# Kernel tuning notes

Hardware: AMD Instinct MI355X
Metric: run time of the kernel (lower is better)

## Reference

```python
import jax, jax.numpy as jnp
import numpy as np

N = 50000      # num_nodes
E = 800000     # num_edges
D_IN = 128
D_HID = 128
D_EMB = 128
G = 4          # num_gcns
BN_EPS = 1e-5


def setup_inputs() -> dict:
    key = jax.random.key(0)
    ks = jax.random.split(key, 8)
    x = jax.random.normal(ks[0], (N, D_IN), dtype=jnp.float32)
    edge_index = jax.random.randint(ks[1], (2, E), 0, N, dtype=jnp.int64)
    # per-GCN params, stacked on leading G axis
    W1 = jax.random.normal(ks[2], (G, D_IN, D_HID), dtype=jnp.float32) / np.sqrt(D_IN)
    b1 = jnp.zeros((G, D_HID), dtype=jnp.float32)
    W2 = jax.random.normal(ks[3], (G, D_HID, D_EMB), dtype=jnp.float32) / np.sqrt(D_HID)
    b2 = jnp.zeros((G, D_EMB), dtype=jnp.float32)
    gamma1 = jnp.ones((G, D_HID), dtype=jnp.float32)
    beta1 = jnp.zeros((G, D_HID), dtype=jnp.float32)
    gamma2 = jnp.ones((G, D_EMB), dtype=jnp.float32)
    beta2 = jnp.zeros((G, D_EMB), dtype=jnp.float32)
    alpha = jnp.asarray(0.25, dtype=jnp.float32)  # PReLU (single shared param)
    mix_embed = jnp.full((N, G), 1.0 / G, dtype=jnp.float32)
    return {"x": x, "edge_index": edge_index, "W1": W1, "b1": b1, "W2": W2,
            "b2": b2, "gamma1": gamma1, "beta1": beta1, "gamma2": gamma2,
            "beta2": beta2, "alpha": alpha, "mix_embed": mix_embed}


def _gcn_norm(edge_index, num_nodes):
    # PyG GCNConv: add self-loops, symmetric normalization D^-1/2 (A+I) D^-1/2
    row, col = edge_index[0], edge_index[1]
    loop = jnp.arange(num_nodes, dtype=edge_index.dtype)
    row = jnp.concatenate([row, loop])
    col = jnp.concatenate([col, loop])
    w = jnp.ones(row.shape[0], dtype=jnp.float32)
    deg = jax.ops.segment_sum(w, col, num_segments=num_nodes)
    dinv = jnp.where(deg > 0, deg ** -0.5, 0.0)
    norm = dinv[row] * w * dinv[col]
    return row, col, norm


def _propagate(h, row, col, norm, num_nodes):
    # gather from source, scale by edge norm, scatter-add to target
    msg = h[row] * norm[:, None]
    return jax.ops.segment_sum(msg, col, num_segments=num_nodes)


def _batchnorm(z, gamma, beta):
    mu = jnp.mean(z, axis=0)
    var = jnp.mean((z - mu) ** 2, axis=0)  # biased, as torch BN training mode
    return (z - mu) * jax.lax.rsqrt(var + BN_EPS) * gamma + beta


def _prelu(z, alpha):
    return jnp.where(z > 0, z, alpha * z)


def reference(x, edge_index, W1, b1, W2, b2, gamma1, beta1, gamma2, beta2, alpha, mix_embed):
    num_nodes = x.shape[0]
    row, col, norm = _gcn_norm(edge_index, num_nodes)
    mix = jax.nn.softmax(mix_embed, axis=-1)  # [N, G]
    out = jnp.zeros((num_nodes, D_EMB), dtype=x.dtype)
    for g in range(G):  # small fixed number of mixture components
        h = x @ W1[g]
        z = _propagate(h, row, col, norm, num_nodes) + b1[g]
        z = _prelu(_batchnorm(z, gamma1[g], beta1[g]), alpha)
        h = z @ W2[g]
        z = _propagate(h, row, col, norm, num_nodes) + b2[g]
        z = _prelu(_batchnorm(z, gamma2[g], beta2[g]), alpha)
        out = out + mix[:, g:g + 1] * z
    return out
```

## Files before the change

kernel.cpp:

```cpp
#include <hip/hip_runtime.h>
#include <stdint.h>

static constexpr float EPS = 1e-5f;
static constexpr int XB = 64;

typedef __attribute__((ext_vector_type(8))) short bfrag;
typedef __attribute__((ext_vector_type(4))) float ffrag;

__device__ __forceinline__ float bf2f(unsigned short u){
  union { unsigned int i; float f; } v; v.i = ((unsigned int)u) << 16; return v.f;
}
__device__ __forceinline__ unsigned short f2bf(float f){
  union { float f; unsigned int i; } v; v.f = f;
  unsigned int x = v.i;
  x += 0x7fffu + ((x >> 16) & 1u);
  return (unsigned short)(x >> 16);
}
__device__ __forceinline__ float lo16(unsigned int v){ return bf2f((unsigned short)(v & 0xffffu)); }
__device__ __forceinline__ float hi16(unsigned int v){ return bf2f((unsigned short)(v >> 16)); }
__device__ __forceinline__ unsigned int pack2(float a, float b){
  return ((unsigned int)f2bf(b) << 16) | (unsigned int)f2bf(a);
}

__global__ __launch_bounds__(256) void k_deg(const int* __restrict__ col, int* __restrict__ indeg,
                                             int N, int E, int dbl,
                                             const float* __restrict__ W1, const float* __restrict__ W2,
                                             unsigned short* __restrict__ Wt1, unsigned short* __restrict__ Wt2){
  int b = blockIdx.x;
  if (b < dbl){
    int e0 = (b * 256 + threadIdx.x) * 2;
    if (e0 < E){
      if (e0 + 1 < E){
        int2 cc = *(const int2*)&col[e0];
        unsigned c0 = (unsigned)cc.x, c1 = (unsigned)cc.y;
        if (c0 < (unsigned)N) atomicAdd(&indeg[c0], 1);
        if (c1 < (unsigned)N) atomicAdd(&indeg[c1], 1);
      } else {
        unsigned c0 = (unsigned)col[e0];
        if (c0 < (unsigned)N) atomicAdd(&indeg[c0], 1);
      }
    }
  } else {
    int idx = (b - dbl) * 256 + threadIdx.x;
    const float* W = W1; unsigned short* Wt = Wt1;
    if (idx >= 65536){ idx -= 65536; W = W2; Wt = Wt2; }
    int c = idx >> 7, k = idx & 127;
    int g = c >> 7, j = c & 127;
    Wt[(size_t)c * 128 + k] = f2bf(W[(size_t)g*16384 + k*128 + j]);
  }
}

__global__ void k_alloc(const int* __restrict__ indeg, int* __restrict__ ctr,
                        int* __restrict__ offs, int* __restrict__ cursor,
                        float* __restrict__ dinv, int N){
  int tid = blockIdx.x * 256 + threadIdx.x;
  int lane = threadIdx.x & 63;
  int v = (tid < N) ? indeg[tid] : 0;
  int incl = v;
  #pragma unroll
  for (int d = 1; d < 64; d <<= 1){
    int u = __shfl_up(incl, d);
    if (lane >= d) incl += u;
  }
  int base = 0;
  if (lane == 63) base = atomicAdd(ctr, incl);
  base = __shfl(base, 63);
  if (tid < N){
    int o = base + incl - v;
    offs[tid] = o; cursor[tid] = o;
    dinv[tid] = rsqrtf((float)(v + 1));
  }
}

__global__ __launch_bounds__(256) void k_scatter(const int* __restrict__ row, const int* __restrict__ col,
                                                 int* __restrict__ cursor, int* __restrict__ csr,
                                                 int N, int E, int sbl,
                                                 const float* __restrict__ x, const float* __restrict__ dinv,
                                                 unsigned short* __restrict__ xs, int total4x){
  int b = blockIdx.x;
  if (b < sbl){
    int e0 = (b * 256 + threadIdx.x) * 2;
    #pragma unroll
    for (int q = 0; q < 2; q++){
      int e = e0 + q;
      if (e < E){
        unsigned c = (unsigned)col[e];
        if (c < (unsigned)N){
          int p = atomicAdd(&cursor[c], 1);
          unsigned r = (unsigned)row[e];
          csr[p] = (r < (unsigned)N) ? (int)r : 0;
        }
      }
    }
  } else {
    int idx = (b - sbl) * 256 + threadIdx.x;
    int stride = (gridDim.x - sbl) * 256;
    for (; idx < total4x; idx += stride){
      int i = idx >> 5;
      float di = dinv[i];
      float4 v = ((const float4*)x)[idx];
      ushort4 o;
      o.x = f2bf(di * v.x); o.y = f2bf(di * v.y);
      o.z = f2bf(di * v.z); o.w = f2bf(di * v.w);
      ((ushort4*)xs)[idx] = o;
    }
  }
}

__global__ __launch_bounds__(256) void k_prop_x(const unsigned int* __restrict__ xs2,
                                               const int* __restrict__ csr,
                                               const int* __restrict__ offs, const int* __restrict__ indeg,
                                               const float* __restrict__ dinv,
                                               unsigned int* __restrict__ s2, int N){
  int i = blockIdx.x * 4 + (threadIdx.x >> 6);
  if (i >= N) return;
  int c2 = threadIdx.x & 63;
  unsigned int sv = xs2[(size_t)i*64 + c2];
  float ax = lo16(sv), ay = hi16(sv);
  int e = offs[i], end = e + indeg[i];
  for (; e + 16 <= end; e += 16){
    int r[16];
    #pragma unroll
    for (int j = 0; j < 16; j++) r[j] = csr[e + j];
    unsigned int v[16];
    #pragma unroll
    for (int j = 0; j < 16; j++) v[j] = xs2[(size_t)r[j]*64 + c2];
    #pragma unroll
    for (int j = 0; j < 16; j++){ ax += lo16(v[j]); ay += hi16(v[j]); }
  }
  for (; e + 4 <= end; e += 4){
    int r0 = csr[e], r1 = csr[e+1], r2 = csr[e+2], r3 = csr[e+3];
    unsigned int v0 = xs2[(size_t)r0*64 + c2], v1 = xs2[(size_t)r1*64 + c2];
    unsigned int v2 = xs2[(size_t)r2*64 + c2], v3 = xs2[(size_t)r3*64 + c2];
    ax += lo16(v0)+lo16(v1)+lo16(v2)+lo16(v3);
    ay += hi16(v0)+hi16(v1)+hi16(v2)+hi16(v3);
  }
  for (; e < end; e++){
    unsigned int v = xs2[(size_t)csr[e]*64 + c2];
    ax += lo16(v); ay += hi16(v);
  }
  float di = dinv[i];
  s2[(size_t)i*64 + c2] = pack2(di * ax, di * ay);
}

__global__ __launch_bounds__(256) void k_gram(const unsigned short* __restrict__ in,
                                              int rstride, int coff128,
                                              float* __restrict__ Gpart, float* __restrict__ msumbase,
                                              int N){
  int gy = blockIdx.y;
  const unsigned short* src = in + gy * coff128;
  float* Gp = Gpart + ((size_t)gy * XB + blockIdx.x) * 16384;
  float* msum = msumbase + gy * 128;

  __shared__ unsigned short st[128 * 40];
  __shared__ float colsum[128];

  int t = threadIdx.x;
  int wv = t >> 6, lane = t & 63, l16 = lane & 15, quad = lane >> 4;
  if (t < 128) colsum[t] = 0.f;

  int sn = t & 31, scb = t >> 5;

  ffrag acc[2][8];
  #pragma unroll
  for (int a = 0; a < 2; a++)
    #pragma unroll
    for (int b = 0; b < 8; b++) acc[a][b] = (ffrag){0.f,0.f,0.f,0.f};

  float cs[16];
  #pragma unroll
  for (int j = 0; j < 16; j++) cs[j] = 0.f;

  for (int c0 = blockIdx.x * 32; c0 < N; c0 += gridDim.x * 32){
    __syncthreads();
    int n = c0 + sn;
    ushort4 u0, u1, u2, u3;
    if (n < N){
      const ushort4* p = (const ushort4*)(src + (size_t)n * rstride + scb * 16);
      u0 = p[0]; u1 = p[1]; u2 = p[2]; u3 = p[3];
    } else {
      u0 = u1 = u2 = u3 = (ushort4){0,0,0,0};
    }
    unsigned short vals[16] = {u0.x,u0.y,u0.z,u0.w, u1.x,u1.y,u1.z,u1.w,
                               u2.x,u2.y,u2.z,u2.w, u3.x,u3.y,u3.z,u3.w};
    #pragma unroll
    for (int j = 0; j < 16; j++){
      st[(scb * 16 + j) * 40 + sn] = vals[j];
      cs[j] += bf2f(vals[j]);
    }
    __syncthreads();
    #pragma unroll
    for (int ta = 0; ta < 2; ta++){
      int ra = wv * 2 + ta;
      bfrag af = *(const bfrag*)&st[(ra * 16 + l16) * 40 + quad * 8];
      #pragma unroll
      for (int tb = 0; tb < 8; tb++){
        bfrag bf = *(const bfrag*)&st[(tb * 16 + l16) * 40 + quad * 8];
        acc[ta][tb] = __builtin_amdgcn_mfma_f32_16x16x32_bf16(af, bf, acc[ta][tb], 0, 0, 0);
      }
    }
  }
  #pragma unroll
  for (int j = 0; j < 16; j++) atomicAdd(&colsum[scb * 16 + j], cs[j]);
  __syncthreads();
  if (t < 128) atomicAdd(&msum[t], colsum[t]);
  #pragma unroll
  for (int ta = 0; ta < 2; ta++){
    #pragma unroll
    for (int tb = 0; tb < 8; tb++){
      int row0 = wv * 32 + ta * 16 + quad * 4;
      int colg = tb * 16 + l16;
      #pragma unroll
      for (int r = 0; r < 4; r++)
        Gp[(size_t)(row0 + r) * 128 + colg] = acc[ta][tb][r];
    }
  }
}

__global__ __launch_bounds__(256) void k_gred(const float* __restrict__ Gpart, float* __restrict__ G){
  int i = blockIdx.x * 256 + threadIdx.x;
  int grp = blockIdx.y;
  const float* src = Gpart + (size_t)grp * XB * 16384;
  float s = 0.f;
  #pragma unroll 4
  for (int xb = 0; xb < XB; xb++) s += src[(size_t)xb * 16384 + i];
  G[(size_t)grp * 16384 + i] = s;
}

__global__ __launch_bounds__(64) void k_bnfit(const float* __restrict__ W,
                                              const float* __restrict__ gamma, const float* __restrict__ beta,
                                              const float* __restrict__ Gbase, int gmul,
                                              const float* __restrict__ msumbase, int mmul,
                                              float* __restrict__ scale, float* __restrict__ shiftF,
                                              float invN){
  int c = blockIdx.x;
  int g = c >> 7, j = c & 127;
  const float* Wc = W + (size_t)g * 16384 + j;
  const float* G  = Gbase + (size_t)g * gmul;
  const float* mv = msumbase + g * mmul;
  __shared__ float wl[128];
  __shared__ float ml[128];
  int t = threadIdx.x;
  for (int k = t; k < 128; k += 64){ wl[k] = Wc[(size_t)k * 128]; ml[k] = mv[k] * invN; }
  __syncthreads();
  float quad = 0.f, dm = 0.f;
  #pragma unroll
  for (int kk = 0; kk < 2; kk++){
    int k = t + kk * 64;
    float wk = wl[k];
    dm += ml[k] * wk;
    const float* Gr = G + (size_t)k * 128;
    float p = 0.f;
    for (int jj = 0; jj < 128; jj += 4){
      float4 gg = *(const float4*)(Gr + jj);
      float4 ww = *(const float4*)(wl + jj);
      p += gg.x*ww.x + gg.y*ww.y + gg.z*ww.z + gg.w*ww.w;
    }
    quad += wk * p;
  }
  for (int o = 32; o > 0; o >>= 1){
    quad += __shfl_down(quad, o);
    dm   += __shfl_down(dm, o);
  }
  if (t == 0){
    float var = quad * invN - dm * dm;
    float sc = gamma[c] * rsqrtf(var + EPS);
    scale[c] = sc;
    shiftF[c] = beta[c] - dm * sc;
  }
}

__global__ __launch_bounds__(256) void k_mm1f(const unsigned short* __restrict__ in,
                                              const unsigned short* __restrict__ Wt,
                                              const float* __restrict__ scale, const float* __restrict__ shiftF,
                                              const float* __restrict__ alpha_p, const float* __restrict__ dinv,
                                              unsigned short* __restrict__ h, int N){
  float alpha = alpha_p[0];
  int wave = threadIdx.x >> 6, lane = threadIdx.x & 63;
  int l16 = lane & 15, quad = lane >> 4;
  int node0 = blockIdx.x * 32 + l16;
  int node1 = node0 + 16;
  int nc0 = node0 < N ? node0 : N - 1;
  int nc1 = node1 < N ? node1 : N - 1;
  int colbase0 = wave * 128;
  float di0 = dinv[nc0], di1 = dinv[nc1];

  const unsigned short* ir0 = in + (size_t)nc0 * 128 + quad * 8;
  const unsigned short* ir1 = in + (size_t)nc1 * 128 + quad * 8;
  bfrag b0a = *(const bfrag*)(ir0),      b0b = *(const bfrag*)(ir1);
  bfrag b1a = *(const bfrag*)(ir0 + 32), b1b = *(const bfrag*)(ir1 + 32);
  bfrag b2a = *(const bfrag*)(ir0 + 64), b2b = *(const bfrag*)(ir1 + 64);
  bfrag b3a = *(const bfrag*)(ir0 + 96), b3b = *(const bfrag*)(ir1 + 96);

  #pragma unroll
  for (int ct = 0; ct < 8; ct++){
    int colbase = colbase0 + ct * 16;
    const unsigned short* wrow = Wt + (size_t)(colbase + l16) * 128 + quad * 8;
    bfrag a0 = *(const bfrag*)(wrow);
    bfrag a1 = *(const bfrag*)(wrow + 32);
    bfrag a2 = *(const bfrag*)(wrow + 64);
    bfrag a3 = *(const bfrag*)(wrow + 96);
    ffrag acc0 = {0.f,0.f,0.f,0.f}, acc1 = {0.f,0.f,0.f,0.f};
    acc0 = __builtin_amdgcn_mfma_f32_16x16x32_bf16(a0, b0a, acc0, 0, 0, 0);
    acc1 = __builtin_amdgcn_mfma_f32_16x16x32_bf16(a0, b0b, acc1, 0, 0, 0);
    acc0 = __builtin_amdgcn_mfma_f32_16x16x32_bf16(a1, b1a, acc0, 0, 0, 0);
    acc1 = __builtin_amdgcn_mfma_f32_16x16x32_bf16(a1, b1b, acc1, 0, 0, 0);
    acc0 = __builtin_amdgcn_mfma_f32_16x16x32_bf16(a2, b2a, acc0, 0, 0, 0);
    acc1 = __builtin_amdgcn_mfma_f32_16x16x32_bf16(a2, b2b, acc1, 0, 0, 0);
    acc0 = __builtin_amdgcn_mfma_f32_16x16x32_bf16(a3, b3a, acc0, 0, 0, 0);
    acc1 = __builtin_amdgcn_mfma_f32_16x16x32_bf16(a3, b3b, acc1, 0, 0, 0);
    int cb = colbase + quad * 4;
    float4 sc = *(const float4*)(scale + cb);
    float4 sh = *(const float4*)(shiftF + cb);
    float v0 = acc0[0]*sc.x + sh.x; v0 = v0 > 0.f ? v0 : alpha*v0;
    float v1 = acc0[1]*sc.y + sh.y; v1 = v1 > 0.f ? v1 : alpha*v1;
    float v2 = acc0[2]*sc.z + sh.z; v2 = v2 > 0.f ? v2 : alpha*v2;
    float v3 = acc0[3]*sc.w + sh.w; v3 = v3 > 0.f ? v3 : alpha*v3;
    float w0 = acc1[0]*sc.x + sh.x; w0 = w0 > 0.f ? w0 : alpha*w0;
    float w1 = acc1[1]*sc.y + sh.y; w1 = w1 > 0.f ? w1 : alpha*w1;
    float w2 = acc1[2]*sc.z + sh.z; w2 = w2 > 0.f ? w2 : alpha*w2;
    float w3 = acc1[3]*sc.w + sh.w; w3 = w3 > 0.f ? w3 : alpha*w3;
    uint2 o0, o1;
    o0.x = pack2(di0*v0, di0*v1); o0.y = pack2(di0*v2, di0*v3);
    o1.x = pack2(di1*w0, di1*w1); o1.y = pack2(di1*w2, di1*w3);
    if (node0 < N) *(uint2*)(h + (size_t)node0 * 512 + cb) = o0;
    if (node1 < N) *(uint2*)(h + (size_t)node1 * 512 + cb) = o1;
  }
}

__global__ __launch_bounds__(256) void k_prop_h(const unsigned int* __restrict__ h2,
                                                const int* __restrict__ csr,
                                                const int* __restrict__ offs, const int* __restrict__ indeg,
                                                const float* __restrict__ dinv,
                                                unsigned int* __restrict__ t2, int N, int coff){
  int i = blockIdx.x * 2 + (threadIdx.x >> 7);
  if (i >= N) return;
  int c2 = coff + (threadIdx.x & 127);
  unsigned int sv = h2[(size_t)i*256 + c2];
  float ax = lo16(sv), ay = hi16(sv);
  int e = offs[i], end = e + indeg[i];
  for (; e + 16 <= end; e += 16){
    int r[16];
    #pragma unroll
    for (int j = 0; j < 16; j++) r[j] = csr[e + j];
    unsigned int v[16];
    #pragma unroll
    for (int j = 0; j < 16; j++) v[j] = h2[(size_t)r[j]*256 + c2];
    #pragma unroll
    for (int j = 0; j < 16; j++){ ax += lo16(v[j]); ay += hi16(v[j]); }
  }
  for (; e + 4 <= end; e += 4){
    int r0 = csr[e], r1 = csr[e+1], r2 = csr[e+2], r3 = csr[e+3];
    unsigned int v0 = h2[(size_t)r0*256 + c2], v1 = h2[(size_t)r1*256 + c2];
    unsigned int v2 = h2[(size_t)r2*256 + c2], v3 = h2[(size_t)r3*256 + c2];
    ax += lo16(v0)+lo16(v1)+lo16(v2)+lo16(v3);
    ay += hi16(v0)+hi16(v1)+hi16(v2)+hi16(v3);
  }
  for (; e < end; e++){
    unsigned int v = h2[(size_t)csr[e]*256 + c2];
    ax += lo16(v); ay += hi16(v);
  }
  float di = dinv[i];
  t2[(size_t)i*256 + c2] = pack2(di * ax, di * ay);
}

__global__ __launch_bounds__(256) void k_mm2f(const unsigned short* __restrict__ t,
                                              const unsigned short* __restrict__ Wt,
                                              const float* __restrict__ scale, const float* __restrict__ shiftF,
                                              const float* __restrict__ alpha_p, const float* __restrict__ mixe,
                                              float* __restrict__ out, int N){
  __shared__ float red[4][16][132];
  float alpha = alpha_p[0];
  int wave = threadIdx.x >> 6, lane = threadIdx.x & 63;
  int l16 = lane & 15, quad = lane >> 4;
  int node = blockIdx.x * 16 + l16;
  int nc = node < N ? node : N - 1;

  float4 me = ((const float4*)mixe)[nc];
  float mx = fmaxf(fmaxf(me.x, me.y), fmaxf(me.z, me.w));
  float e0 = __expf(me.x - mx), e1 = __expf(me.y - mx), e2 = __expf(me.z - mx), e3 = __expf(me.w - mx);
  float inv = 1.f / (e0 + e1 + e2 + e3);
  float wvx = ((wave == 0) ? e0 : (wave == 1) ? e1 : (wave == 2) ? e2 : e3) * inv;

  const unsigned short* inrow = t + (size_t)nc * 512 + wave * 128 + quad * 8;
  bfrag b0 = *(const bfrag*)(inrow);
  bfrag b1 = *(const bfrag*)(inrow + 32);
  bfrag b2 = *(const bfrag*)(inrow + 64);
  bfrag b3 = *(const bfrag*)(inrow + 96);

  #pragma unroll
  for (int ct = 0; ct < 8; ct++){
    int c512 = wave * 128 + ct * 16;
    const unsigned short* wrow = Wt + (size_t)(c512 + l16) * 128 + quad * 8;
    bfrag a0 = *(const bfrag*)(wrow);
    bfrag a1 = *(const bfrag*)(wrow + 32);
    bfrag a2 = *(const bfrag*)(wrow + 64);
    bfrag a3 = *(const bfrag*)(wrow + 96);
    ffrag acc = {0.f, 0.f, 0.f, 0.f};
    acc = __builtin_amdgcn_mfma_f32_16x16x32_bf16(a0, b0, acc, 0, 0, 0);
    acc = __builtin_amdgcn_mfma_f32_16x16x32_bf16(a1, b1, acc, 0, 0, 0);
    acc = __builtin_amdgcn_mfma_f32_16x16x32_bf16(a2, b2, acc, 0, 0, 0);
    acc = __builtin_amdgcn_mfma_f32_16x16x32_bf16(a3, b3, acc, 0, 0, 0);
    int cb = c512 + quad * 4;
    float4 sc = *(const float4*)(scale + cb);
    float4 sh = *(const float4*)(shiftF + cb);
    float v0 = acc[0]*sc.x + sh.x; v0 = v0 > 0.f ? v0 : alpha*v0;
    float v1 = acc[1]*sc.y + sh.y; v1 = v1 > 0.f ? v1 : alpha*v1;
    float v2 = acc[2]*sc.z + sh.z; v2 = v2 > 0.f ? v2 : alpha*v2;
    float v3 = acc[3]*sc.w + sh.w; v3 = v3 > 0.f ? v3 : alpha*v3;
    int j = ct * 16 + quad * 4;
    float4 wr = {wvx*v0, wvx*v1, wvx*v2, wvx*v3};
    *(float4*)&red[wave][l16][j] = wr;
  }
  __syncthreads();
  int tt = threadIdx.x;
  int nn = tt >> 4, j0 = (tt & 15) * 8;
  int gnode = blockIdx.x * 16 + nn;
  if (gnode < N){
    float4 r0 = {0,0,0,0}, r1 = {0,0,0,0};
    #pragma unroll
    for (int w = 0; w < 4; w++){
      float4 p0 = *(const float4*)&red[w][nn][j0];
      float4 p1 = *(const float4*)&red[w][nn][j0 + 4];
      r0.x += p0.x; r0.y += p0.y; r0.z += p0.z; r0.w += p0.w;
      r1.x += p1.x; r1.y += p1.y; r1.z += p1.z; r1.w += p1.w;
    }
    float* op = out + (size_t)gnode * 128 + j0;
    *(float4*)(op) = r0;
    *(float4*)(op + 4) = r1;
  }
}

extern "C" void kernel_launch(void* const* d_in, const int* in_sizes, int n_in,
                              void* d_out, int out_size, void* d_ws, size_t ws_size,
                              hipStream_t stream) {
  const float* x      = (const float*)d_in[0];
  const int*   ei     = (const int*)d_in[1];
  const float* W1     = (const float*)d_in[2];
  const float* W2     = (const float*)d_in[4];
  const float* gamma1 = (const float*)d_in[6];
  const float* beta1  = (const float*)d_in[7];
  const float* gamma2 = (const float*)d_in[8];
  const float* beta2  = (const float*)d_in[9];
  const float* alpha  = (const float*)d_in[10];
  const float* mixe   = (const float*)d_in[11];
  float* out = (float*)d_out;

  const int N = in_sizes[0] / 128;
  const int E = in_sizes[1] / 2;
  const int* rowv = ei;
  const int* colv = ei + E;

  char* w = (char*)d_ws;
  size_t off = 0;
  auto take = [&](size_t bytes) -> void* {
    void* p = w + off;
    off = (off + bytes + 255) & ~(size_t)255;
    return p;
  };
  size_t zbeg = off;
  int*   indeg  = (int*)take((size_t)N * 4);
  int*   ctr    = (int*)take(256);
  float* m1     = (float*)take(512);
  float* m2     = (float*)take(2048);
  size_t zend = off;
  float* G1     = (float*)take(65536);
  float* G2     = (float*)take(262144);
  float* Gpart  = (float*)take((size_t)4 * XB * 16384 * 4);
  int*   cursor = (int*)take((size_t)N * 4);
  int*   offs   = (int*)take((size_t)N * 4);
  float* dinv   = (float*)take((size_t)N * 4);
  float* scale1 = (float*)take(2048);
  float* shift1 = (float*)take(2048);
  float* scale2 = (float*)take(2048);
  float* shift2 = (float*)take(2048);
  int*   csr    = (int*)take((size_t)E * 4);
  unsigned short* Wt1 = (unsigned short*)take(512 * 128 * 2);
  unsigned short* Wt2 = (unsigned short*)take(512 * 128 * 2);
  unsigned short* xs = (unsigned short*)take((size_t)N * 128 * 2);
  unsigned short* sb = (unsigned short*)take((size_t)N * 128 * 2);
  unsigned short* h  = (unsigned short*)take((size_t)N * 512 * 2);
  unsigned short* tb = (unsigned short*)take((size_t)N * 512 * 2);

  hipMemsetAsync((char*)d_ws + zbeg, 0, zend - zbeg, stream);

  int nb  = (N + 255) / 256;
  int dbl = (E + 511) / 512;
  float invN = 1.0f / (float)N;

  k_deg<<<dbl + 512, 256, 0, stream>>>(colv, indeg, N, E, dbl, W1, W2, Wt1, Wt2);
  k_alloc<<<nb, 256, 0, stream>>>(indeg, ctr, offs, cursor, dinv, N);
  k_scatter<<<dbl + 1024, 256, 0, stream>>>(rowv, colv, cursor, csr, N, E, dbl, x, dinv, xs, N * 32);

  k_prop_x<<<(N + 3) / 4, 256, 0, stream>>>((const unsigned int*)xs, csr, offs, indeg, dinv, (unsigned int*)sb, N);

  k_gram<<<dim3(XB, 1), 256, 0, stream>>>(sb, 128, 0, Gpart, m1, N);
  k_gred<<<dim3(64, 1), 256, 0, stream>>>(Gpart, G1);
  k_bnfit<<<512, 64, 0, stream>>>(W1, gamma1, beta1, G1, 0, m1, 0, scale1, shift1, invN);
  k_mm1f<<<(N + 31) / 32, 256, 0, stream>>>(sb, Wt1, scale1, shift1, alpha, dinv, h, N);

  k_prop_h<<<(N + 1) / 2, 256, 0, stream>>>((const unsigned int*)h, csr, offs, indeg, dinv, (unsigned int*)tb, N, 0);
  k_prop_h<<<(N + 1) / 2, 256, 0, stream>>>((const unsigned int*)h, csr, offs, indeg, dinv, (unsigned int*)tb, N, 128);

  k_gram<<<dim3(XB, 4), 256, 0, stream>>>(tb, 512, 128, Gpart, m2, N);
  k_gred<<<dim3(64, 4), 256, 0, stream>>>(Gpart, G2);
  k_bnfit<<<512, 64, 0, stream>>>(W2, gamma2, beta2, G2, 16384, m2, 128, scale2, shift2, invN);
  k_mm2f<<<(N + 15) / 16, 256, 0, stream>>>(tb, Wt2, scale2, shift2, alpha, mixe, out, N);
}
```

Measured before the change: 552.7 us.

## Privatize degree histogram and CSR cursors into 8 copies, merge prop_h launches

Degree counting and CSR scatter now use eight per-block-group private histograms and cursors, which spreads atomic contention across separate copies. The alloc kernel sums the copies, writes a total degree array, and derives a per-copy cursor base. Edge loads are widened to int4, four edges per thread. The two half-channel k_prop_h launches are replaced by one launch with one 256-thread block per node covering all 512 channels, trading more scratch memory and memset for fewer atomic collisions and launches.

```diff
diff --git a/kernel.cpp b/kernel.cpp
--- a/kernel.cpp
+++ b/kernel.cpp
@@ -28,16 +28,19 @@
                                              unsigned short* __restrict__ Wt1, unsigned short* __restrict__ Wt2){
   int b = blockIdx.x;
   if (b < dbl){
-    int e0 = (b * 256 + threadIdx.x) * 2;
-    if (e0 < E){
-      if (e0 + 1 < E){
-        int2 cc = *(const int2*)&col[e0];
-        unsigned c0 = (unsigned)cc.x, c1 = (unsigned)cc.y;
-        if (c0 < (unsigned)N) atomicAdd(&indeg[c0], 1);
-        if (c1 < (unsigned)N) atomicAdd(&indeg[c1], 1);
-      } else {
-        unsigned c0 = (unsigned)col[e0];
-        if (c0 < (unsigned)N) atomicAdd(&indeg[c0], 1);
+    int* hist = indeg + (size_t)(b & 7) * N;
+    int e0 = (b * 256 + threadIdx.x) * 4;
+    if (e0 + 4 <= E){
+      int4 cc = *(const int4*)&col[e0];
+      unsigned c0 = (unsigned)cc.x, c1 = (unsigned)cc.y, c2 = (unsigned)cc.z, c3 = (unsigned)cc.w;
+      if (c0 < (unsigned)N) atomicAdd(&hist[c0], 1);
+      if (c1 < (unsigned)N) atomicAdd(&hist[c1], 1);
+      if (c2 < (unsigned)N) atomicAdd(&hist[c2], 1);
+      if (c3 < (unsigned)N) atomicAdd(&hist[c3], 1);
+    } else {
+      for (int e = e0; e < E; e++){
+        unsigned c = (unsigned)col[e];
+        if (c < (unsigned)N) atomicAdd(&hist[c], 1);
       }
     }
   } else {
@@ -52,10 +55,18 @@
 
 __global__ void k_alloc(const int* __restrict__ indeg, int* __restrict__ ctr,
                         int* __restrict__ offs, int* __restrict__ cursor,
-                        float* __restrict__ dinv, int N){
+                        int* __restrict__ deg, float* __restrict__ dinv, int N){
   int tid = blockIdx.x * 256 + threadIdx.x;
   int lane = threadIdx.x & 63;
-  int v = (tid < N) ? indeg[tid] : 0;
+  int vs[8];
+  int v = 0;
+  if (tid < N){
+    #pragma unroll
+    for (int s = 0; s < 8; s++){ vs[s] = indeg[(size_t)s * N + tid]; v += vs[s]; }
+  } else {
+    #pragma unroll
+    for (int s = 0; s < 8; s++) vs[s] = 0;
+  }
   int incl = v;
   #pragma unroll
   for (int d = 1; d < 64; d <<= 1){
@@ -67,7 +78,11 @@
   base = __shfl(base, 63);
   if (tid < N){
     int o = base + incl - v;
-    offs[tid] = o; cursor[tid] = o;
+    offs[tid] = o;
+    deg[tid] = v;
+    int run = o;
+    #pragma unroll
+    for (int s = 0; s < 8; s++){ cursor[(size_t)s * N + tid] = run; run += vs[s]; }
     dinv[tid] = rsqrtf((float)(v + 1));
   }
 }
@@ -79,14 +94,26 @@
                                                  unsigned short* __restrict__ xs, int total4x){
   int b = blockIdx.x;
   if (b < sbl){
-    int e0 = (b * 256 + threadIdx.x) * 2;
-    #pragma unroll
-    for (int q = 0; q < 2; q++){
-      int e = e0 + q;
-      if (e < E){
+    int* cur = cursor + (size_t)(b & 7) * N;
+    int e0 = (b * 256 + threadIdx.x) * 4;
+    if (e0 + 4 <= E){
+      int4 cc = *(const int4*)&col[e0];
+      int4 rr = *(const int4*)&row[e0];
+      unsigned c0 = (unsigned)cc.x, c1 = (unsigned)cc.y, c2 = (unsigned)cc.z, c3 = (unsigned)cc.w;
+      int p0 = -1, p1 = -1, p2 = -1, p3 = -1;
+      if (c0 < (unsigned)N) p0 = atomicAdd(&cur[c0], 1);
+      if (c1 < (unsigned)N) p1 = atomicAdd(&cur[c1], 1);
+      if (c2 < (unsigned)N) p2 = atomicAdd(&cur[c2], 1);
+      if (c3 < (unsigned)N) p3 = atomicAdd(&cur[c3], 1);
+      if (p0 >= 0) csr[p0] = ((unsigned)rr.x < (unsigned)N) ? rr.x : 0;
+      if (p1 >= 0) csr[p1] = ((unsigned)rr.y < (unsigned)N) ? rr.y : 0;
+      if (p2 >= 0) csr[p2] = ((unsigned)rr.z < (unsigned)N) ? rr.z : 0;
+      if (p3 >= 0) csr[p3] = ((unsigned)rr.w < (unsigned)N) ? rr.w : 0;
+    } else {
+      for (int e = e0; e < E; e++){
         unsigned c = (unsigned)col[e];
         if (c < (unsigned)N){
-          int p = atomicAdd(&cursor[c], 1);
+          int p = atomicAdd(&cur[c], 1);
           unsigned r = (unsigned)row[e];
           csr[p] = (r < (unsigned)N) ? (int)r : 0;
         }
@@ -109,7 +136,7 @@
 
 __global__ __launch_bounds__(256) void k_prop_x(const unsigned int* __restrict__ xs2,
                                                const int* __restrict__ csr,
-                                               const int* __restrict__ offs, const int* __restrict__ indeg,
+                                               const int* __restrict__ offs, const int* __restrict__ deg,
                                                const float* __restrict__ dinv,
                                                unsigned int* __restrict__ s2, int N){
   int i = blockIdx.x * 4 + (threadIdx.x >> 6);
@@ -117,7 +144,7 @@
   int c2 = threadIdx.x & 63;
   unsigned int sv = xs2[(size_t)i*64 + c2];
   float ax = lo16(sv), ay = hi16(sv);
-  int e = offs[i], end = e + indeg[i];
+  int e = offs[i], end = e + deg[i];
   for (; e + 16 <= end; e += 16){
     int r[16];
     #pragma unroll
@@ -330,15 +357,14 @@
 
 __global__ __launch_bounds__(256) void k_prop_h(const unsigned int* __restrict__ h2,
                                                 const int* __restrict__ csr,
-                                                const int* __restrict__ offs, const int* __restrict__ indeg,
+                                                const int* __restrict__ offs, const int* __restrict__ deg,
                                                 const float* __restrict__ dinv,
-                                                unsigned int* __restrict__ t2, int N, int coff){
-  int i = blockIdx.x * 2 + (threadIdx.x >> 7);
-  if (i >= N) return;
-  int c2 = coff + (threadIdx.x & 127);
+                                                unsigned int* __restrict__ t2, int N){
+  int i = blockIdx.x;
+  int c2 = threadIdx.x;
   unsigned int sv = h2[(size_t)i*256 + c2];
   float ax = lo16(sv), ay = hi16(sv);
-  int e = offs[i], end = e + indeg[i];
+  int e = offs[i], end = e + deg[i];
   for (; e + 16 <= end; e += 16){
     int r[16];
     #pragma unroll
@@ -459,7 +485,7 @@
     return p;
   };
   size_t zbeg = off;
-  int*   indeg  = (int*)take((size_t)N * 4);
+  int*   indeg  = (int*)take((size_t)8 * N * 4);
   int*   ctr    = (int*)take(256);
   float* m1     = (float*)take(512);
   float* m2     = (float*)take(2048);
@@ -467,8 +493,9 @@
   float* G1     = (float*)take(65536);
   float* G2     = (float*)take(262144);
   float* Gpart  = (float*)take((size_t)4 * XB * 16384 * 4);
-  int*   cursor = (int*)take((size_t)N * 4);
+  int*   cursor = (int*)take((size_t)8 * N * 4);
   int*   offs   = (int*)take((size_t)N * 4);
+  int*   deg    = (int*)take((size_t)N * 4);
   float* dinv   = (float*)take((size_t)N * 4);
   float* scale1 = (float*)take(2048);
   float* shift1 = (float*)take(2048);
@@ -485,22 +512,21 @@
   hipMemsetAsync((char*)d_ws + zbeg, 0, zend - zbeg, stream);
 
   int nb  = (N + 255) / 256;
-  int dbl = (E + 511) / 512;
+  int dbl = (E + 1023) / 1024;
   float invN = 1.0f / (float)N;
 
   k_deg<<<dbl + 512, 256, 0, stream>>>(colv, indeg, N, E, dbl, W1, W2, Wt1, Wt2);
-  k_alloc<<<nb, 256, 0, stream>>>(indeg, ctr, offs, cursor, dinv, N);
+  k_alloc<<<nb, 256, 0, stream>>>(indeg, ctr, offs, cursor, deg, dinv, N);
   k_scatter<<<dbl + 1024, 256, 0, stream>>>(rowv, colv, cursor, csr, N, E, dbl, x, dinv, xs, N * 32);
 
-  k_prop_x<<<(N + 3) / 4, 256, 0, stream>>>((const unsigned int*)xs, csr, offs, indeg, dinv, (unsigned int*)sb, N);
+  k_prop_x<<<(N + 3) / 4, 256, 0, stream>>>((const unsigned int*)xs, csr, offs, deg, dinv, (unsigned int*)sb, N);
 
   k_gram<<<dim3(XB, 1), 256, 0, stream>>>(sb, 128, 0, Gpart, m1, N);
   k_gred<<<dim3(64, 1), 256, 0, stream>>>(Gpart, G1);
   k_bnfit<<<512, 64, 0, stream>>>(W1, gamma1, beta1, G1, 0, m1, 0, scale1, shift1, invN);
   k_mm1f<<<(N + 31) / 32, 256, 0, stream>>>(sb, Wt1, scale1, shift1, alpha, dinv, h, N);
 
-  k_prop_h<<<(N + 1) / 2, 256, 0, stream>>>((const unsigned int*)h, csr, offs, indeg, dinv, (unsigned int*)tb, N, 0);
-  k_prop_h<<<(N + 1) / 2, 256, 0, stream>>>((const unsigned int*)h, csr, offs, indeg, dinv, (unsigned int*)tb, N, 128);
+  k_prop_h<<<N, 256, 0, stream>>>((const unsigned int*)h, csr, offs, deg, dinv, (unsigned int*)tb, N);
 
   k_gram<<<dim3(XB, 4), 256, 0, stream>>>(tb, 512, 128, Gpart, m2, N);
   k_gred<<<dim3(64, 4), 256, 0, stream>>>(Gpart, G2);
```

Result: faster. 536.4 us (-3.0%).
